# Kernel tuning notes

Measured on AMD Instinct MI355X. Metric: run time of the kernel, lower is better.

The kernel has to match this reference:

```python
import jax, jax.numpy as jnp
import numpy as np


def setup_inputs() -> dict:
    key = jax.random.key(0)
    k1, k2 = jax.random.split(key)
    B, dim, m, n = 4096, 1024, 128, 128
    inputs = jax.random.normal(k1, (B, dim), dtype=jnp.float32)
    som_weights = jax.random.normal(k2, (m * n, dim), dtype=jnp.float32)
    return {"inputs": inputs, "som_weights": som_weights, "m": m, "n": n, "T": 100}


def reference(inputs, som_weights, m, n, T):
    # Grid locations: [(i, j) for i in range(m) for j in range(n)] -> [m*n, 2]
    ii, jj = jnp.meshgrid(jnp.arange(m), jnp.arange(n), indexing="ij")
    locs = jnp.stack([ii.reshape(-1), jj.reshape(-1)], axis=-1).astype(jnp.float32)  # [mn, 2]

    # Squared L2 distances via the matmul trick (same math as sum((x-w)^2)).
    x2 = jnp.sum(inputs * inputs, axis=1, keepdims=True)        # [B, 1]
    w2 = jnp.sum(som_weights * som_weights, axis=1)             # [mn]
    d2 = x2 - 2.0 * (inputs @ som_weights.T) + w2[None, :]      # [B, mn]

    # BMU search (argmin over codebook).
    bmu = jnp.argmin(d2, axis=1)                                # [B] int
    bmu_loc = locs[bmu]                                         # [B, 2]

    # Manhattan distance on the grid, Gaussian-of-Manhattan influence.
    manh = jnp.sum(jnp.abs(locs[None, :, :] - bmu_loc[:, None, :]), axis=-1)  # [B, mn]
    T2 = jnp.float32(T * T)
    infl = jnp.exp(-(manh * manh) / T2)                         # [B, mn]

    # Original: reduce_sum over (batch, m) then mean over n == total_sum / n.
    loss = jnp.sum(d2 * infl) / jnp.float32(n)
    return loss
```

## Files before the change

kernel.cpp:

```cpp
#include <hip/hip_runtime.h>


typedef __attribute__((ext_vector_type(8))) short short8;
typedef __attribute__((ext_vector_type(16))) float f32x16;
typedef __attribute__((ext_vector_type(2))) long i64x2;
typedef unsigned short ushort_t;

#define B_ROWS 4096
#define DIM    1024
#define MN     16384
#define NJB    128

__device__ static inline ushort_t f32_to_bf16(float f) {
    unsigned u = __float_as_uint(f);
    u = (u + 0x7FFFu + ((u >> 16) & 1u)) >> 16;
    return (ushort_t)u;
}
__device__ static inline float bf16_to_f32(ushort_t h) {
    return __uint_as_float(((unsigned)h) << 16);
}
__device__ static inline void gload_lds16(const void* g, void* l) {
    __builtin_amdgcn_global_load_lds(
        (const __attribute__((address_space(1))) unsigned*)g,
        (__attribute__((address_space(3))) unsigned*)l, 16, 0, 0);
}

__global__ __launch_bounds__(256) void k_convert(
    const float* __restrict__ X, const float* __restrict__ W,
    unsigned char* __restrict__ Xf8, unsigned char* __restrict__ Wf8,
    float* __restrict__ x2, float* __restrict__ w2) {
    int row  = blockIdx.x * 4 + (threadIdx.x >> 6);
    int lane = threadIdx.x & 63;
    const float4* src;
    int* dst;
    float* sq;
    if (row < B_ROWS) {
        src = (const float4*)(X + (size_t)row * DIM);
        dst = (int*)(Xf8 + (size_t)row * DIM);
        sq  = x2 + row;
    } else {
        int r2 = row - B_ROWS;
        src = (const float4*)(W + (size_t)r2 * DIM);
        dst = (int*)(Wf8 + (size_t)r2 * DIM);
        sq  = w2 + r2;
    }
    const int t4 = lane >> 4;
    const int Foff = ((lane >> 3) & 1) * 2 + ((lane >> 1) & 3) * 4 + (lane & 1);
    float s = 0.f;
    #pragma unroll
    for (int c = 0; c < 4; ++c) {
        int F = (c * 4 + t4) * 16 + Foff;
        float4 v = src[F];
        s += v.x * v.x + v.y * v.y + v.z * v.z + v.w * v.w;
        int r = __builtin_amdgcn_cvt_pk_fp8_f32(v.x, v.y, 0, false);
        r     = __builtin_amdgcn_cvt_pk_fp8_f32(v.z, v.w, r, true);
        dst[c * 64 + lane] = r;
    }
    #pragma unroll
    for (int d = 1; d < 64; d <<= 1) s += __shfl_xor(s, d);
    if (lane == 0) *sq = s;
}

__global__ __launch_bounds__(512, 3) void k_gemm(
    const unsigned char* __restrict__ Xf8, const unsigned char* __restrict__ Wf8,
    const float* __restrict__ x2, const float* __restrict__ w2,
    ushort_t* __restrict__ d2, float* __restrict__ pmin, int* __restrict__ pidx) {
    __shared__ __attribute__((aligned(1024))) unsigned char ldsb[65536];

    const int tid  = threadIdx.x;
    const int lane = tid & 63;
    const int w    = tid >> 6;
    const int wrM  = w >> 1;
    const int wcN  = w & 1;
    const int l31  = lane & 31;
    const int h    = lane >> 5;

    const int bid = blockIdx.x;
    const int swz = (bid & 7) * 256 + (bid >> 3);
    const int tn  = swz >> 4;
    const int tm  = swz & 15;
    const int phase = (bid & 7) * 2;

    const size_t aRow = (size_t)tm * 256;
    const size_t bRow = (size_t)tn * 128;

    const unsigned char* srcA0; const unsigned char* srcA1; const unsigned char* srcB0;
    {
        int p, crow, lcol;
        p = tid * 16; crow = p >> 7; lcol = (p & 127) ^ ((crow & 7) << 4);
        srcA0 = Xf8 + (aRow + crow * 2 + (lcol >> 6)) * DIM + (lcol & 63);
        p = 8192 + tid * 16; crow = p >> 7; lcol = (p & 127) ^ ((crow & 7) << 4);
        srcA1 = Xf8 + (aRow + crow * 2 + (lcol >> 6)) * DIM + (lcol & 63);
        p = tid * 16; crow = p >> 7; lcol = (p & 127) ^ ((crow & 7) << 4);
        srcB0 = Wf8 + (bRow + crow * 2 + (lcol >> 6)) * DIM + (lcol & 63);
    }

    #define STAGE(kt, buf) do {                                                  \
        const int _kt = (kt) & 15;                                               \
        gload_lds16(srcA0 + _kt * 64, ldsb + (buf) * 24576 + tid * 16);          \
        gload_lds16(srcA1 + _kt * 64, ldsb + (buf) * 24576 + 8192 + tid * 16);   \
        gload_lds16(srcB0 + _kt * 64, ldsb + (buf) * 24576 + 16384 + tid * 16);  \
    } while (0)

    const int rA0  = wrM * 64 + l31;
    const int rB0  = wcN * 64 + l31;
    const int fb   = (l31 & 1) * 64 + h * 32;
    const int aA0 = (rA0 >> 1) * 128 + ((fb)      ^ (((rA0 >> 1) & 7) << 4));
    const int aA1 = (rA0 >> 1) * 128 + ((fb + 16) ^ (((rA0 >> 1) & 7) << 4));
    const int aB0 = 16384 + (rB0 >> 1) * 128 + ((fb)      ^ (((rB0 >> 1) & 7) << 4));
    const int aB1 = 16384 + (rB0 >> 1) * 128 + ((fb + 16) ^ (((rB0 >> 1) & 7) << 4));

    f32x16 acc[2][2];
    #pragma unroll
    for (int i = 0; i < 2; ++i)
        #pragma unroll
        for (int j = 0; j < 2; ++j) acc[i][j] = (f32x16)0.f;

    #define BAR() __builtin_amdgcn_s_barrier()
    #define SCB() __builtin_amdgcn_sched_barrier(0)

    STAGE(phase, 0);
    STAGE(phase + 1, 1);
    asm volatile("s_waitcnt vmcnt(3)" ::: "memory");
    SCB();
    BAR();

    for (int kt = 0; kt < 16; ++kt) {
        const int bb = (kt & 1) * 24576;
        i64x2 xq0[2], xq1[2], wq0[2], wq1[2];
        #pragma unroll
        for (int mi = 0; mi < 2; ++mi) {
            xq0[mi] = *(const i64x2*)(ldsb + bb + aA0 + mi * 2048);
            xq1[mi] = *(const i64x2*)(ldsb + bb + aA1 + mi * 2048);
        }
        #pragma unroll
        for (int ni = 0; ni < 2; ++ni) {
            wq0[ni] = *(const i64x2*)(ldsb + bb + aB0 + ni * 2048);
            wq1[ni] = *(const i64x2*)(ldsb + bb + aB1 + ni * 2048);
        }
        asm volatile("s_waitcnt lgkmcnt(4)" ::: "memory");
        SCB();
        __builtin_amdgcn_s_setprio(1);
        #pragma unroll
        for (int mi = 0; mi < 2; ++mi)
            #pragma unroll
            for (int ni = 0; ni < 2; ++ni) {
                acc[mi][ni] = __builtin_amdgcn_mfma_f32_32x32x16_fp8_fp8(
                    wq0[ni][0], xq0[mi][0], acc[mi][ni], 0, 0, 0);
                acc[mi][ni] = __builtin_amdgcn_mfma_f32_32x32x16_fp8_fp8(
                    wq0[ni][1], xq0[mi][1], acc[mi][ni], 0, 0, 0);
            }
        __builtin_amdgcn_s_setprio(0);
        asm volatile("s_waitcnt lgkmcnt(0)" ::: "memory");
        SCB();
        __builtin_amdgcn_s_setprio(1);
        #pragma unroll
        for (int mi = 0; mi < 2; ++mi)
            #pragma unroll
            for (int ni = 0; ni < 2; ++ni) {
                acc[mi][ni] = __builtin_amdgcn_mfma_f32_32x32x16_fp8_fp8(
                    wq1[ni][0], xq1[mi][0], acc[mi][ni], 0, 0, 0);
                acc[mi][ni] = __builtin_amdgcn_mfma_f32_32x32x16_fp8_fp8(
                    wq1[ni][1], xq1[mi][1], acc[mi][ni], 0, 0, 0);
            }
        __builtin_amdgcn_s_setprio(0);
        SCB();
        BAR();
        if (kt < 14) {
            STAGE(kt + 2 + phase, kt & 1);
            asm volatile("s_waitcnt vmcnt(3)" ::: "memory");
            SCB();
            BAR();
        } else if (kt == 14) {
            asm volatile("s_waitcnt vmcnt(0)" ::: "memory");
            SCB();
            BAR();
        }
    }

    unsigned char* wls = ldsb + w * 8192;
    const int colw = tn * 128 + wcN * 64;
    const int rowbase = tm * 256 + wrM * 64;
    float4 w2q[2][4];
    #pragma unroll
    for (int ni = 0; ni < 2; ++ni)
        #pragma unroll
        for (int q = 0; q < 4; ++q)
            w2q[ni][q] = *(const float4*)(w2 + colw + ni * 32 + q * 8 + h * 4);

    float mnA[2]; int ixA[2];
    #pragma unroll
    for (int mi = 0; mi < 2; ++mi) {
        const int xr = mi * 32 + l31;
        const float xx = x2[rowbase + xr];
        float mn = __builtin_inff(); int ix = 0x7fffffff;
        #pragma unroll
        for (int ni = 0; ni < 2; ++ni) {
            #pragma unroll
            for (int q = 0; q < 4; ++q) {
                float dv[4];
                ushort4 st;
                #pragma unroll
                for (int t = 0; t < 4; ++t) {
                    dv[t] = xx - 2.f * acc[mi][ni][q * 4 + t] + w2q[ni][q][t];
                    st[t] = (unsigned short)f32_to_bf16(dv[t]);
                }
                *(ushort4*)(wls + xr * 128
                            + ((ni * 64 + q * 16 + h * 8) ^ ((xr & 7) << 4))) = st;
                #pragma unroll
                for (int t = 0; t < 4; ++t) {
                    const int cand = colw + ni * 32 + q * 8 + h * 4 + t;
                    if (dv[t] < mn || (dv[t] == mn && cand < ix)) { mn = dv[t]; ix = cand; }
                }
            }
        }
        float om = __shfl_xor(mn, 32);
        int   oi = __shfl_xor(ix, 32);
        if (om < mn || (om == mn && oi < ix)) { mn = om; ix = oi; }
        mnA[mi] = mn; ixA[mi] = ix;
    }
    asm volatile("s_waitcnt lgkmcnt(0)" ::: "memory");
    SCB();
    #pragma unroll
    for (int j = 0; j < 8; ++j) {
        const int rl = j * 8 + (lane >> 3);
        const int cb = (lane & 7) * 16;
        short8 v = *(const short8*)(wls + rl * 128 + (cb ^ ((rl & 7) << 4)));
        *(short8*)((char*)(d2 + (size_t)(rowbase + rl) * MN + colw) + cb) = v;
    }
    __syncthreads();
    float* smin = (float*)ldsb;
    int*   sidx = (int*)(ldsb + 2048);
    if (lane < 32) {
        #pragma unroll
        for (int mi = 0; mi < 2; ++mi) {
            const int rloc = wrM * 64 + mi * 32 + l31;
            smin[rloc * 2 + wcN] = mnA[mi];
            sidx[rloc * 2 + wcN] = ixA[mi];
        }
    }
    __syncthreads();
    if (tid < 256) {
        float m0 = smin[tid * 2];     int i0 = sidx[tid * 2];
        float m1 = smin[tid * 2 + 1]; int i1 = sidx[tid * 2 + 1];
        bool take1 = (m1 < m0) || (m1 == m0 && i1 < i0);
        const int row = tm * 256 + tid;
        pmin[(size_t)row * NJB + tn] = take1 ? m1 : m0;
        pidx[(size_t)row * NJB + tn] = take1 ? i1 : i0;
    }
    #undef STAGE
    #undef BAR
    #undef SCB
}

__global__ __launch_bounds__(256) void k_loss(
    const ushort_t* __restrict__ d2, const float* __restrict__ pmin,
    const int* __restrict__ pidx, float* __restrict__ lossb) {
    __shared__ float etab[255];
    __shared__ float red[4];
    __shared__ int bmu_s;
    int t = threadIdx.x;
    if (t < 255) etab[t] = __expf(-(float)(t * t) * 1e-4f);
    int row = blockIdx.x;
    if (t < 64) {
        float m0 = pmin[(size_t)row * NJB + t];
        int   i0 = pidx[(size_t)row * NJB + t];
        float m1 = pmin[(size_t)row * NJB + t + 64];
        int   i1 = pidx[(size_t)row * NJB + t + 64];
        if (m1 < m0 || (m1 == m0 && i1 < i0)) { m0 = m1; i0 = i1; }
        #pragma unroll
        for (int d = 1; d < 64; d <<= 1) {
            float om = __shfl_xor(m0, d);
            int   oi = __shfl_xor(i0, d);
            if (om < m0 || (om == m0 && oi < i0)) { m0 = om; i0 = oi; }
        }
        if (t == 0) bmu_s = i0;
    }
    __syncthreads();
    int bl = bmu_s;
    int bi = bl >> 7, bj = bl & 127;
    const ushort_t* dr = d2 + (size_t)row * MN;
    float s = 0.f;
    #pragma unroll
    for (int c = 0; c < 8; ++c) {
        int j = c * 2048 + t * 8;
        short8 v = *(const short8*)&dr[j];
        int di = abs((j >> 7) - bi);
        int jc = j & 127;
        #pragma unroll
        for (int u = 0; u < 8; ++u) {
            int mh = di + abs(jc + u - bj);
            s += bf16_to_f32((ushort_t)v[u]) * etab[mh];
        }
    }
    #pragma unroll
    for (int d = 1; d < 64; d <<= 1) s += __shfl_xor(s, d);
    if ((t & 63) == 0) red[t >> 6] = s;
    __syncthreads();
    if (t == 0) lossb[row] = red[0] + red[1] + red[2] + red[3];
}

__global__ __launch_bounds__(256) void k_final(
    const float* __restrict__ lossb, float* __restrict__ out) {
    __shared__ float red[4];
    int t = threadIdx.x;
    float s = 0.f;
    #pragma unroll
    for (int k = 0; k < 16; ++k) s += lossb[t + k * 256];
    #pragma unroll
    for (int d = 1; d < 64; d <<= 1) s += __shfl_xor(s, d);
    if ((t & 63) == 0) red[t >> 6] = s;
    __syncthreads();
    if (t == 0) out[0] = (red[0] + red[1] + red[2] + red[3]) * (1.0f / 128.0f);
}

extern "C" void kernel_launch(void* const* d_in, const int* in_sizes, int n_in,
                              void* d_out, int out_size, void* d_ws, size_t ws_size,
                              hipStream_t stream) {
    const float* X = (const float*)d_in[0];
    const float* W = (const float*)d_in[1];
    unsigned char* ws = (unsigned char*)d_ws;
    unsigned char* Xf8 = ws;
    unsigned char* Wf8 = ws + 4194304;
    float*    x2   = (float*)(ws + 20971520);
    float*    w2   = (float*)(ws + 20987904);
    ushort_t* d2   = (ushort_t*)(ws + 21053440);
    float*    pmin = (float*)(ws + 155271168);
    int*      pidx = (int*)(ws + 157368320);
    float*    lossb= (float*)(ws + 159465472);

    k_convert<<<5120, 256, 0, stream>>>(X, W, Xf8, Wf8, x2, w2);
    k_gemm<<<2048, 512, 0, stream>>>(Xf8, Wf8, x2, w2, d2, pmin, pidx);
    k_loss<<<4096, 256, 0, stream>>>(d2, pmin, pidx, lossb);
    k_final<<<1, 256, 0, stream>>>(lossb, (float*)d_out);
}
```

Measured before the change: 161.6 us.

## Switch GEMM K-loop to triple-buffered LDS with one barrier per iteration

Moves the fp8 GEMM main loop from double to triple buffering in LDS, so the global-to-LDS prefetch for step kt+2 is issued right after the fragment reads. This removes one of the two block barriers per K iteration and fully unrolls the loop. It also drops the per-block phase rotation of the K start offset. LDS use grows from 64 KB to 72 KB per block, which may lower occupancy below the launch-bounds target of 3 blocks per CU.

```diff
diff --git a/kernel.cpp b/kernel.cpp
--- a/kernel.cpp
+++ b/kernel.cpp
@@ -65,7 +65,7 @@
     const unsigned char* __restrict__ Xf8, const unsigned char* __restrict__ Wf8,
     const float* __restrict__ x2, const float* __restrict__ w2,
     ushort_t* __restrict__ d2, float* __restrict__ pmin, int* __restrict__ pidx) {
-    __shared__ __attribute__((aligned(1024))) unsigned char ldsb[65536];
+    __shared__ __attribute__((aligned(1024))) unsigned char ldsb[73728];
 
     const int tid  = threadIdx.x;
     const int lane = tid & 63;
@@ -79,7 +79,6 @@
     const int swz = (bid & 7) * 256 + (bid >> 3);
     const int tn  = swz >> 4;
     const int tm  = swz & 15;
-    const int phase = (bid & 7) * 2;
 
     const size_t aRow = (size_t)tm * 256;
     const size_t bRow = (size_t)tn * 128;
@@ -95,11 +94,10 @@
         srcB0 = Wf8 + (bRow + crow * 2 + (lcol >> 6)) * DIM + (lcol & 63);
     }
 
-    #define STAGE(kt, buf) do {                                                  \
-        const int _kt = (kt) & 15;                                               \
-        gload_lds16(srcA0 + _kt * 64, ldsb + (buf) * 24576 + tid * 16);          \
-        gload_lds16(srcA1 + _kt * 64, ldsb + (buf) * 24576 + 8192 + tid * 16);   \
-        gload_lds16(srcB0 + _kt * 64, ldsb + (buf) * 24576 + 16384 + tid * 16);  \
+    #define STAGE(kt, bb) do {                                                   \
+        gload_lds16(srcA0 + (kt) * 64, ldsb + (bb) + tid * 16);                  \
+        gload_lds16(srcA1 + (kt) * 64, ldsb + (bb) + 8192 + tid * 16);           \
+        gload_lds16(srcB0 + (kt) * 64, ldsb + (bb) + 16384 + tid * 16);          \
     } while (0)
 
     const int rA0  = wrM * 64 + l31;
@@ -119,14 +117,16 @@
     #define BAR() __builtin_amdgcn_s_barrier()
     #define SCB() __builtin_amdgcn_sched_barrier(0)
 
-    STAGE(phase, 0);
-    STAGE(phase + 1, 1);
+    STAGE(0, 0);
+    STAGE(1, 24576);
     asm volatile("s_waitcnt vmcnt(3)" ::: "memory");
     SCB();
     BAR();
 
+    #pragma unroll
     for (int kt = 0; kt < 16; ++kt) {
-        const int bb = (kt & 1) * 24576;
+        const int bb = (kt % 3) * 24576;
+        const int bs = ((kt + 2) % 3) * 24576;
         i64x2 xq0[2], xq1[2], wq0[2], wq1[2];
         #pragma unroll
         for (int mi = 0; mi < 2; ++mi) {
@@ -138,6 +138,7 @@
             wq0[ni] = *(const i64x2*)(ldsb + bb + aB0 + ni * 2048);
             wq1[ni] = *(const i64x2*)(ldsb + bb + aB1 + ni * 2048);
         }
+        if (kt < 14) STAGE(kt + 2, bs);
         asm volatile("s_waitcnt lgkmcnt(4)" ::: "memory");
         SCB();
         __builtin_amdgcn_s_setprio(1);
@@ -165,17 +166,10 @@
             }
         __builtin_amdgcn_s_setprio(0);
         SCB();
+        if (kt < 14)       asm volatile("s_waitcnt vmcnt(3)" ::: "memory");
+        else if (kt == 14) asm volatile("s_waitcnt vmcnt(0)" ::: "memory");
+        SCB();
         BAR();
-        if (kt < 14) {
-            STAGE(kt + 2 + phase, kt & 1);
-            asm volatile("s_waitcnt vmcnt(3)" ::: "memory");
-            SCB();
-            BAR();
-        } else if (kt == 14) {
-            asm volatile("s_waitcnt vmcnt(0)" ::: "memory");
-            SCB();
-            BAR();
-        }
     }
 
     unsigned char* wls = ldsb + w * 8192;
```

New measurement: 195.7 us. 21.1% more time.
